# Kernel tuning notes

Measured on AMD Instinct MI355X. Metric: run time of the kernel, lower is better.

Reference implementation:

```python
import jax, jax.numpy as jnp
import numpy as np

B, T, HID, H = 4, 2048, 768, 12
D = HID // H  # head_dim = 64


def setup_inputs() -> dict:
    key = jax.random.key(0)
    ks = jax.random.split(key, 8)
    s = 0.02  # keep logits in a sane range
    return {
        "hidden_states": jax.random.normal(ks[0], (B, T, HID), dtype=jnp.float32),
        "attention_mask": jax.random.normal(ks[1], (B, 1, 1, T), dtype=jnp.float32),
        "Wq": jax.random.normal(ks[2], (HID, HID), dtype=jnp.float32) * s,
        "bq": jax.random.normal(ks[3], (HID,), dtype=jnp.float32) * s,
        "Wk": jax.random.normal(ks[4], (HID, HID), dtype=jnp.float32) * s,
        "bk": jax.random.normal(ks[5], (HID,), dtype=jnp.float32) * s,
        "Wv": jax.random.normal(ks[6], (HID, HID), dtype=jnp.float32) * s,
        "bv": jax.random.normal(ks[7], (HID,), dtype=jnp.float32) * s,
    }


def _split_heads(x):
    # [B, T, HID] -> [B, H, T, D]
    b, t, _ = x.shape
    return x.reshape(b, t, H, D).transpose(0, 2, 1, 3)


def reference(hidden_states, attention_mask, Wq, bq, Wk, bk, Wv, bv):
    # nn.Linear: y = x @ W^T + b
    q = _split_heads(hidden_states @ Wq.T + bq)  # [B,H,T,D]
    k = _split_heads(hidden_states @ Wk.T + bk)
    v = _split_heads(hidden_states @ Wv.T + bv)

    scores = jnp.einsum("bhqd,bhkd->bhqk", q, k) / jnp.sqrt(jnp.float32(D))
    causal = jnp.tril(jnp.ones((T, T), dtype=bool))[None, None]  # [1,1,T,T]
    neg_inf = jnp.finfo(scores.dtype).min
    scores = jnp.where(causal, scores, neg_inf)
    # attention_mask here is a float additive mask (randn: min<0, max>1 branch)
    scores = scores + attention_mask

    probs = jax.nn.softmax(scores, axis=-1)  # [B,H,T,T]
    ctx = jnp.einsum("bhqk,bhkd->bhqd", probs, v)  # [B,H,T,D]
    return ctx.transpose(0, 2, 1, 3).reshape(B, T, HID)
```

## Files before the change

kernel.cpp:

```cpp
#include <hip/hip_runtime.h>
#include <hip/hip_bf16.h>
#include <stdint.h>

typedef __attribute__((ext_vector_type(8))) short short8x;
typedef __attribute__((ext_vector_type(4))) float float4x;
typedef __attribute__((ext_vector_type(2))) unsigned int uint2x;

#define B_SZ 4
#define T_SEQ 2048
#define HID_SZ 768
#define NH 12
#define HD 64
#define LDP 72
#define QBLK 64
#define NT 32
#define LOG2E 1.4426950408889634f
#define SCL2 0.18033688011112043f

__device__ __forceinline__ unsigned short f2b(float f) {
    union { float f; unsigned int u; } v; v.f = f;
    unsigned int u = v.u;
    u += 0x7fffu + ((u >> 16) & 1u);
    return (unsigned short)(u >> 16);
}

__device__ __forceinline__ unsigned int pkbf(float a, float b) {
    __hip_bfloat162 p = __float22bfloat162_rn(make_float2(a, b));
    return *(unsigned int*)&p;
}

__global__ __launch_bounds__(256) void qkv_gemm(
    const float* __restrict__ X,
    const float* __restrict__ Wq, const float* __restrict__ bq,
    const float* __restrict__ Wk, const float* __restrict__ bk,
    const float* __restrict__ Wv, const float* __restrict__ bv,
    unsigned short* __restrict__ Yq, unsigned short* __restrict__ Yk,
    unsigned short* __restrict__ Yv)
{
    const int z = blockIdx.z;
    const float* W    = (z == 0) ? Wq : (z == 1) ? Wk : Wv;
    const float* bias = (z == 0) ? bq : (z == 1) ? bk : bv;
    unsigned short* Y = (z == 0) ? Yq : (z == 1) ? Yk : Yv;

    __shared__ unsigned short As[128 * LDP];
    __shared__ unsigned short Bs[128 * LDP];
    const int tid  = threadIdx.x;
    const int lane = tid & 63;
    const int w    = tid >> 6;
    const int bm = blockIdx.x, bn = blockIdx.y;
    const int wm = (w >> 1) * 64, wn = (w & 1) * 64;
    const int lr = lane & 15;
    const int hi = lane >> 4;

    float4x acc[4][4];
#pragma unroll
    for (int i = 0; i < 4; ++i)
#pragma unroll
        for (int j = 0; j < 4; ++j) acc[i][j] = (float4x)0.0f;

    for (int k0 = 0; k0 < HID_SZ; k0 += 64) {
        __syncthreads();
#pragma unroll
        for (int i = 0; i < 8; ++i) {
            int f4 = tid + i * 256;
            int row = f4 >> 4, c4 = f4 & 15;
            float4 va = *(const float4*)(X + (size_t)(bm * 128 + row) * HID_SZ + k0 + c4 * 4);
            uint2x ua; ua.x = pkbf(va.x, va.y); ua.y = pkbf(va.z, va.w);
            *(uint2x*)&As[row * LDP + c4 * 4] = ua;
            float4 vb = *(const float4*)(W + (size_t)(bn * 128 + row) * HID_SZ + k0 + c4 * 4);
            uint2x ub; ub.x = pkbf(vb.x, vb.y); ub.y = pkbf(vb.z, vb.w);
            *(uint2x*)&Bs[row * LDP + c4 * 4] = ub;
        }
        __syncthreads();

        short8x a[4][2], bf[4][2];
#pragma unroll
        for (int rf = 0; rf < 4; ++rf)
#pragma unroll
            for (int ks = 0; ks < 2; ++ks)
                a[rf][ks] = *(const short8x*)&As[(wm + rf * 16 + lr) * LDP + ks * 32 + hi * 8];
#pragma unroll
        for (int cf = 0; cf < 4; ++cf)
#pragma unroll
            for (int ks = 0; ks < 2; ++ks)
                bf[cf][ks] = *(const short8x*)&Bs[(wn + cf * 16 + lr) * LDP + ks * 32 + hi * 8];
        __builtin_amdgcn_s_setprio(1);
#pragma unroll
        for (int rf = 0; rf < 4; ++rf)
#pragma unroll
            for (int cf = 0; cf < 4; ++cf)
#pragma unroll
                for (int ks = 0; ks < 2; ++ks)
                    acc[rf][cf] = __builtin_amdgcn_mfma_f32_16x16x32_bf16(
                        a[rf][ks], bf[cf][ks], acc[rf][cf], 0, 0, 0);
        __builtin_amdgcn_s_setprio(0);
    }

#pragma unroll
    for (int rf = 0; rf < 4; ++rf)
#pragma unroll
        for (int cf = 0; cf < 4; ++cf) {
            int n = bn * 128 + wn + cf * 16 + lr;
            float bv = bias[n];
            int h = n >> 6, d = n & 63;
#pragma unroll
            for (int reg = 0; reg < 4; ++reg) {
                int m = bm * 128 + wm + rf * 16 + hi * 4 + reg;
                int b = m >> 11, t = m & 2047;
                Y[(((size_t)b * NH + h) * T_SEQ + t) * HD + d] = f2b(acc[rf][cf][reg] + bv);
            }
        }
}

__global__ __launch_bounds__(256) void attn(
    const unsigned short* __restrict__ Q, const unsigned short* __restrict__ K,
    const unsigned short* __restrict__ V, const float* __restrict__ mask,
    float* __restrict__ out)
{
    __shared__ unsigned short Vt[2][HD * LDP];
    __shared__ unsigned short Ps[4][16 * LDP];
    __shared__ unsigned short Msb[T_SEQ];

    const int tid = threadIdx.x, lane = tid & 63, w = tid >> 6;
    const int lr = lane & 15, hi = lane >> 4;
    const int bh = blockIdx.x;
    const int jj = NT - 1 - blockIdx.y;
    const int b = bh / NH, h = bh % NH;
    const size_t base = (size_t)bh * T_SEQ * HD;
    const int q0 = jj * QBLK;

    {
        int t8 = tid * 8;
        float4 m0 = *(const float4*)&mask[b * T_SEQ + t8];
        float4 m1 = *(const float4*)&mask[b * T_SEQ + t8 + 4];
        uint2x u0, u1;
        u0.x = pkbf(m0.x * LOG2E, m0.y * LOG2E);
        u0.y = pkbf(m0.z * LOG2E, m0.w * LOG2E);
        u1.x = pkbf(m1.x * LOG2E, m1.y * LOG2E);
        u1.y = pkbf(m1.z * LOG2E, m1.w * LOG2E);
        *(uint2x*)&Msb[t8]     = u0;
        *(uint2x*)&Msb[t8 + 4] = u1;
    }

    const int c8 = tid & 7;
    const int kk0 = (tid >> 3) * 2;
    const int prk = kk0 ^ (c8 << 3);

    short8x qa[2];
#pragma unroll
    for (int ks = 0; ks < 2; ++ks)
        qa[ks] = *(const short8x*)(Q + base + (size_t)(q0 + w * 16 + lr) * HD + ks * 32 + hi * 8);

    float4x o[4];
    float lp = 0.0f;
#pragma unroll
    for (int j = 0; j < 4; ++j) o[j] = (float4x)0.0f;

    {
        short8x v0 = *(const short8x*)(V + base + (size_t)kk0 * HD + c8 * 8);
        short8x v1 = *(const short8x*)(V + base + (size_t)(kk0 + 1) * HD + c8 * 8);
#pragma unroll
        for (int j = 0; j < 8; ++j) {
            unsigned pk = ((unsigned)(unsigned short)v0[j]) |
                          (((unsigned)(unsigned short)v1[j]) << 16);
            *(unsigned*)&Vt[0][(c8 * 8 + j) * LDP + prk] = pk;
        }
    }
    __syncthreads();

    int cur = 0;
    int kv = 0;
    short8x kb0[4][2], kb1[4][2];
#pragma unroll
    for (int c = 0; c < 4; ++c)
#pragma unroll
        for (int ks = 0; ks < 2; ++ks)
            kb0[c][ks] = *(const short8x*)(K + base + (size_t)(c * 16 + lr) * HD + ks * 32 + hi * 8);

    auto body = [&](short8x (&kb)[4][2], short8x (&kbn)[4][2]) -> bool {
        const bool pf = (kv < jj);
        short8x nv0, nv1;
        if (pf) {
#pragma unroll
            for (int c = 0; c < 4; ++c)
#pragma unroll
                for (int ks = 0; ks < 2; ++ks)
                    kbn[c][ks] = *(const short8x*)(K + base + (size_t)((kv + 1) * 64 + c * 16 + lr) * HD + ks * 32 + hi * 8);
            nv0 = *(const short8x*)(V + base + (size_t)((kv + 1) * 64 + kk0) * HD + c8 * 8);
            nv1 = *(const short8x*)(V + base + (size_t)((kv + 1) * 64 + kk0 + 1) * HD + c8 * 8);
        }

        float4x s[4];
        __builtin_amdgcn_s_setprio(1);
#pragma unroll
        for (int c = 0; c < 4; ++c) {
            s[c] = (float4x)0.0f;
#pragma unroll
            for (int ks = 0; ks < 2; ++ks)
                s[c] = __builtin_amdgcn_mfma_f32_16x16x32_bf16(
                    kb[c][ks], qa[ks], s[c], 0, 0, 0);
        }
        __builtin_amdgcn_s_setprio(0);

        const bool diag = (kv == jj);
        const int qloc = w * 16 + lr;
        float ps = 0.0f;
#pragma unroll
        for (int c = 0; c < 4; ++c) {
            uint2x mv = *(const uint2x*)&Msb[kv * 64 + c * 16 + hi * 4];
            float mf[4];
            mf[0] = __uint_as_float(mv.x << 16);
            mf[1] = __uint_as_float(mv.x & 0xffff0000u);
            mf[2] = __uint_as_float(mv.y << 16);
            mf[3] = __uint_as_float(mv.y & 0xffff0000u);
#pragma unroll
            for (int reg = 0; reg < 4; ++reg) {
                float x = s[c][reg] * SCL2 + mf[reg];
                if (diag) {
                    int kloc = c * 16 + hi * 4 + reg;
                    if (kloc > qloc) x = -1.0e30f;
                }
                float p = exp2f(x);
                s[c][reg] = p;
                ps += p;
            }
        }
        lp += ps;

#pragma unroll
        for (int c = 0; c < 4; ++c) {
            uint2x pk;
            pk.x = pkbf(s[c][0], s[c][1]);
            pk.y = pkbf(s[c][2], s[c][3]);
            *(uint2x*)&Ps[w][lr * LDP + c * 16 + hi * 4] = pk;
        }

        short8x pa[2], vb[4][2];
#pragma unroll
        for (int ks = 0; ks < 2; ++ks)
            pa[ks] = *(const short8x*)&Ps[w][lr * LDP + ks * 32 + hi * 8];
#pragma unroll
        for (int cf = 0; cf < 4; ++cf)
#pragma unroll
            for (int ks = 0; ks < 2; ++ks) {
                int d = cf * 16 + lr;
                int pcb = (ks * 32 + hi * 8) ^ (((d >> 3) & 7) << 3);
                vb[cf][ks] = *(const short8x*)&Vt[cur][d * LDP + pcb];
            }
        __builtin_amdgcn_s_setprio(1);
#pragma unroll
        for (int cf = 0; cf < 4; ++cf)
#pragma unroll
            for (int ks = 0; ks < 2; ++ks)
                o[cf] = __builtin_amdgcn_mfma_f32_16x16x32_bf16(
                    vb[cf][ks], pa[ks], o[cf], 0, 0, 0);
        __builtin_amdgcn_s_setprio(0);

        if (pf) {
            int nxt = cur ^ 1;
#pragma unroll
            for (int j = 0; j < 8; ++j) {
                unsigned pk = ((unsigned)(unsigned short)nv0[j]) |
                              (((unsigned)(unsigned short)nv1[j]) << 16);
                *(unsigned*)&Vt[nxt][(c8 * 8 + j) * LDP + prk] = pk;
            }
            __syncthreads();
            cur = nxt;
        }
        ++kv;
        return pf;
    };

    while (true) {
        if (!body(kb0, kb1)) break;
        if (!body(kb1, kb0)) break;
    }

    float lsum = lp;
    lsum += __shfl_xor(lsum, 16, 64);
    lsum += __shfl_xor(lsum, 32, 64);
    float inv = 1.0f / lsum;

    int t = q0 + w * 16 + lr;
#pragma unroll
    for (int cf = 0; cf < 4; ++cf) {
        float4 st;
        st.x = o[cf][0] * inv; st.y = o[cf][1] * inv;
        st.z = o[cf][2] * inv; st.w = o[cf][3] * inv;
        *(float4*)(out + ((size_t)b * T_SEQ + t) * HID_SZ + h * HD + cf * 16 + hi * 4) = st;
    }
}

extern "C" void kernel_launch(void* const* d_in, const int* in_sizes, int n_in,
                              void* d_out, int out_size, void* d_ws, size_t ws_size,
                              hipStream_t stream) {
    const float* X    = (const float*)d_in[0];
    const float* mask = (const float*)d_in[1];
    const float* Wq   = (const float*)d_in[2];
    const float* bq   = (const float*)d_in[3];
    const float* Wk   = (const float*)d_in[4];
    const float* bk   = (const float*)d_in[5];
    const float* Wv   = (const float*)d_in[6];
    const float* bv   = (const float*)d_in[7];
    float* out = (float*)d_out;

    unsigned short* qw = (unsigned short*)d_ws;
    unsigned short* kw = qw + (size_t)B_SZ * T_SEQ * HID_SZ;
    unsigned short* vw = kw + (size_t)B_SZ * T_SEQ * HID_SZ;

    dim3 blk(256);
    qkv_gemm<<<dim3(64, 6, 3), blk, 0, stream>>>(X, Wq, bq, Wk, bk, Wv, bv, qw, kw, vw);
    attn<<<dim3(48, NT), blk, 0, stream>>>(qw, kw, vw, mask, out);
}
```

Measured before the change: 176.9 us.

## Write V transposed from projection and read it directly in attention

The projection kernel now writes V in a [B,H,D,T] transposed layout (packed 4-wide stores when z==2). The attention kernel reads these V fragments straight from global memory instead of staging and transposing V through double-buffered shared memory. This removes the per-iteration shared-memory transpose and the block-wide __syncthreads. In exchange, V loads now sit directly on the MFMA critical path without prefetch, and the K register double-buffering is replaced by a single buffer reloaded after QK.

```diff
diff --git a/kernel.cpp b/kernel.cpp
--- a/kernel.cpp
+++ b/kernel.cpp
@@ -103,21 +103,27 @@
             int n = bn * 128 + wn + cf * 16 + lr;
             float bv = bias[n];
             int h = n >> 6, d = n & 63;
-#pragma unroll
-            for (int reg = 0; reg < 4; ++reg) {
-                int m = bm * 128 + wm + rf * 16 + hi * 4 + reg;
-                int b = m >> 11, t = m & 2047;
-                Y[(((size_t)b * NH + h) * T_SEQ + t) * HD + d] = f2b(acc[rf][cf][reg] + bv);
+            int m0 = bm * 128 + wm + rf * 16 + hi * 4;
+            int b = m0 >> 11, t0 = m0 & 2047;
+            if (z == 2) {
+                uint2x pk;
+                pk.x = pkbf(acc[rf][cf][0] + bv, acc[rf][cf][1] + bv);
+                pk.y = pkbf(acc[rf][cf][2] + bv, acc[rf][cf][3] + bv);
+                *(uint2x*)&Y[(((size_t)b * NH + h) * HD + d) * T_SEQ + t0] = pk;
+            } else {
+#pragma unroll
+                for (int reg = 0; reg < 4; ++reg)
+                    Y[(((size_t)b * NH + h) * T_SEQ + t0 + reg) * HD + d] =
+                        f2b(acc[rf][cf][reg] + bv);
             }
         }
 }
 
 __global__ __launch_bounds__(256) void attn(
     const unsigned short* __restrict__ Q, const unsigned short* __restrict__ K,
-    const unsigned short* __restrict__ V, const float* __restrict__ mask,
+    const unsigned short* __restrict__ VT, const float* __restrict__ mask,
     float* __restrict__ out)
 {
-    __shared__ unsigned short Vt[2][HD * LDP];
     __shared__ unsigned short Ps[4][16 * LDP];
     __shared__ unsigned short Msb[T_SEQ];
 
@@ -126,7 +132,8 @@
     const int bh = blockIdx.x;
     const int jj = NT - 1 - blockIdx.y;
     const int b = bh / NH, h = bh % NH;
-    const size_t base = (size_t)bh * T_SEQ * HD;
+    const size_t base  = (size_t)bh * T_SEQ * HD;
+    const size_t vbase = (size_t)bh * HD * T_SEQ;
     const int q0 = jj * QBLK;
 
     {
@@ -142,10 +149,6 @@
         *(uint2x*)&Msb[t8 + 4] = u1;
     }
 
-    const int c8 = tid & 7;
-    const int kk0 = (tid >> 3) * 2;
-    const int prk = kk0 ^ (c8 << 3);
-
     short8x qa[2];
 #pragma unroll
     for (int ks = 0; ks < 2; ++ks)
@@ -156,40 +159,16 @@
 #pragma unroll
     for (int j = 0; j < 4; ++j) o[j] = (float4x)0.0f;
 
-    {
-        short8x v0 = *(const short8x*)(V + base + (size_t)kk0 * HD + c8 * 8);
-        short8x v1 = *(const short8x*)(V + base + (size_t)(kk0 + 1) * HD + c8 * 8);
-#pragma unroll
-        for (int j = 0; j < 8; ++j) {
-            unsigned pk = ((unsigned)(unsigned short)v0[j]) |
-                          (((unsigned)(unsigned short)v1[j]) << 16);
-            *(unsigned*)&Vt[0][(c8 * 8 + j) * LDP + prk] = pk;
-        }
-    }
     __syncthreads();
 
-    int cur = 0;
-    int kv = 0;
-    short8x kb0[4][2], kb1[4][2];
+    short8x kb[4][2];
 #pragma unroll
     for (int c = 0; c < 4; ++c)
 #pragma unroll
         for (int ks = 0; ks < 2; ++ks)
-            kb0[c][ks] = *(const short8x*)(K + base + (size_t)(c * 16 + lr) * HD + ks * 32 + hi * 8);
-
-    auto body = [&](short8x (&kb)[4][2], short8x (&kbn)[4][2]) -> bool {
-        const bool pf = (kv < jj);
-        short8x nv0, nv1;
-        if (pf) {
-#pragma unroll
-            for (int c = 0; c < 4; ++c)
-#pragma unroll
-                for (int ks = 0; ks < 2; ++ks)
-                    kbn[c][ks] = *(const short8x*)(K + base + (size_t)((kv + 1) * 64 + c * 16 + lr) * HD + ks * 32 + hi * 8);
-            nv0 = *(const short8x*)(V + base + (size_t)((kv + 1) * 64 + kk0) * HD + c8 * 8);
-            nv1 = *(const short8x*)(V + base + (size_t)((kv + 1) * 64 + kk0 + 1) * HD + c8 * 8);
-        }
-
+            kb[c][ks] = *(const short8x*)(K + base + (size_t)(c * 16 + lr) * HD + ks * 32 + hi * 8);
+
+    for (int kv = 0; kv <= jj; ++kv) {
         float4x s[4];
         __builtin_amdgcn_s_setprio(1);
 #pragma unroll
@@ -201,6 +180,14 @@
                     kb[c][ks], qa[ks], s[c], 0, 0, 0);
         }
         __builtin_amdgcn_s_setprio(0);
+
+        if (kv < jj) {
+#pragma unroll
+            for (int c = 0; c < 4; ++c)
+#pragma unroll
+                for (int ks = 0; ks < 2; ++ks)
+                    kb[c][ks] = *(const short8x*)(K + base + (size_t)((kv + 1) * 64 + c * 16 + lr) * HD + ks * 32 + hi * 8);
+        }
 
         const bool diag = (kv == jj);
         const int qloc = w * 16 + lr;
@@ -235,18 +222,18 @@
             *(uint2x*)&Ps[w][lr * LDP + c * 16 + hi * 4] = pk;
         }
 
-        short8x pa[2], vb[4][2];
+        short8x vb[4][2];
+#pragma unroll
+        for (int cf = 0; cf < 4; ++cf)
+#pragma unroll
+            for (int ks = 0; ks < 2; ++ks)
+                vb[cf][ks] = *(const short8x*)(VT + vbase + (size_t)(cf * 16 + lr) * T_SEQ + kv * 64 + ks * 32 + hi * 8);
+
+        short8x pa[2];
 #pragma unroll
         for (int ks = 0; ks < 2; ++ks)
             pa[ks] = *(const short8x*)&Ps[w][lr * LDP + ks * 32 + hi * 8];
-#pragma unroll
-        for (int cf = 0; cf < 4; ++cf)
-#pragma unroll
-            for (int ks = 0; ks < 2; ++ks) {
-                int d = cf * 16 + lr;
-                int pcb = (ks * 32 + hi * 8) ^ (((d >> 3) & 7) << 3);
-                vb[cf][ks] = *(const short8x*)&Vt[cur][d * LDP + pcb];
-            }
+
         __builtin_amdgcn_s_setprio(1);
 #pragma unroll
         for (int cf = 0; cf < 4; ++cf)
@@ -255,25 +242,6 @@
                 o[cf] = __builtin_amdgcn_mfma_f32_16x16x32_bf16(
                     vb[cf][ks], pa[ks], o[cf], 0, 0, 0);
         __builtin_amdgcn_s_setprio(0);
-
-        if (pf) {
-            int nxt = cur ^ 1;
-#pragma unroll
-            for (int j = 0; j < 8; ++j) {
-                unsigned pk = ((unsigned)(unsigned short)nv0[j]) |
-                              (((unsigned)(unsigned short)nv1[j]) << 16);
-                *(unsigned*)&Vt[nxt][(c8 * 8 + j) * LDP + prk] = pk;
-            }
-            __syncthreads();
-            cur = nxt;
-        }
-        ++kv;
-        return pf;
-    };
-
-    while (true) {
-        if (!body(kb0, kb1)) break;
-        if (!body(kb1, kb0)) break;
     }
 
     float lsum = lp;
```

Result: slower. 254.8 us (+44.0%).
